# Kernel tuning notes

Measured on AMD Instinct MI355X. Metric: run time of the kernel, lower is better.

## Reference

```python
import jax, jax.numpy as jnp
import numpy as np

B, N, L, K = 32, 512, 8, 8


def setup_inputs() -> dict:
    key = jax.random.key(0)
    k1, k2 = jax.random.split(key)
    A = jax.random.normal(k1, (B, N, N), dtype=jnp.float32)
    A = 0.5 * (A + A.transpose(0, 2, 1))  # symmetric matrix, as in MMF use-case
    O_stack = jax.random.normal(k2, (L, B, K, K), dtype=jnp.float32)  # per-level KxK rotations
    rng = np.random.default_rng(0)
    idx = np.stack([np.sort(rng.choice(N, K, replace=False)) for _ in range(B * L)])
    indices = jnp.asarray(idx.reshape(B, L, K), dtype=jnp.int32)  # sorted, distinct per (b,l)
    wavelet = indices[:, :, 0]  # wavelet index is one of the selected indices per level
    return {"A": A, "O_stack": O_stack, "indices": indices, "wavelet": wavelet}


def reference(A, O_stack, indices, wavelet):
    Bz, Nz, _ = A.shape
    Lz = O_stack.shape[0]
    eye = jnp.eye(Nz, dtype=A.dtype)

    def build_U(idx, O):
        # identity except the KxK block at (idx_i, idx_j) replaced by O
        # (matches torch boolean-mask row-major fill since idx is sorted)
        return eye.at[idx[:, None], idx[None, :]].set(O)

    right = None
    for l in range(Lz):
        U = jax.vmap(build_U)(indices[:, l], O_stack[l])  # [B,N,N]
        right = U if l == 0 else U @ right
        A = U @ A @ U.transpose(0, 2, 1)

    # final masking: zero rows/cols of wavelet indices, keep diagonal
    active = jnp.ones((Bz, Nz), dtype=A.dtype).at[jnp.arange(Bz)[:, None], wavelet].set(0.0)
    left = active[:, :, None] * active[:, None, :]
    d = jnp.arange(Nz)
    left = left.at[:, d, d].set(1.0)
    D = A * left
    A_rec = right.transpose(0, 2, 1) @ D @ right
    return (A_rec, right, D)
```

## Files before the change

kernel.cpp:

```cpp
#include <hip/hip_runtime.h>

#define BATCH 32
#define NDIM 512
#define LNUM 8
#define KDIM 8

#define WS_PM     0
#define WS_ACT    640
#define WS_RAT    78976
#define WS_RDT    111744
#define WS_STRIDE 144512

#define LSTR 65
typedef float f4 __attribute__((ext_vector_type(4)));

__global__ __launch_bounds__(256) void k_prep(
    const float* __restrict__ A, const float* __restrict__ O,
    const int* __restrict__ indices, const int* __restrict__ wavelet,
    float* __restrict__ ws, float* __restrict__ out)
{
    const int b  = blockIdx.x;
    const int cy = blockIdx.y;
    const int tid = threadIdx.x;
    float* base = ws + (size_t)b * WS_STRIDE;
    const size_t seg = (size_t)BATCH*NDIM*NDIM;

    __shared__ float Wl[64*LSTR];
    __shared__ __align__(16) float Buf1[64*LSTR];
    __shared__ __align__(16) float Buf2[64*LSTR];
    __shared__ __align__(16) float Buf3[64*LSTR];
    __shared__ int   pml[NDIM];
    __shared__ float actl[NDIM];
    __shared__ float actS[64];
    __shared__ int   idxsh[64];
    __shared__ int   Ssh[64];
    __shared__ float Oall[LNUM*KDIM*KDIM];
    __shared__ int   s_sh;

    for (int t = tid; t < LNUM*KDIM*KDIM; t += 256) {
        int l = t >> 6, k = t & 63;
        Oall[t] = O[((size_t)l*BATCH + b)*(KDIM*KDIM) + k];
    }
    if (tid < 64) idxsh[tid] = indices[b*64 + tid];
    for (int n = tid; n < NDIM; n += 256) { pml[n] = -1; actl[n] = 1.f; }
    __syncthreads();

    const int wv = tid >> 6;
    const int ln = tid & 63;
    int s_reg = 0;

    if (wv == 0) {
        int n = idxsh[ln];
        bool first = true;
        for (int t = 0; t < ln; ++t) if (idxsh[t] == n) first = false;
        unsigned long long m = __ballot(first);
        int rank = __popcll(m & ((1ull << ln) - 1ull));
        s_reg = (int)__popcll(m);
        if (first) { pml[n] = rank; Ssh[rank] = n; }
        if (ln >= s_reg) Ssh[ln] = 0;
        if (ln < LNUM) actl[wavelet[b*LNUM + ln]] = 0.f;
        if (ln == 0) s_sh = s_reg;
    }
    __syncthreads();

    if (wv == 0) {
        actS[ln] = actl[Ssh[ln]];
        for (int rr = 0; rr < 64; ++rr)
            Wl[rr*LSTR + ln] = (rr == ln && rr < s_reg) ? 1.f : 0.f;
        for (int l = 0; l < LNUM; ++l) {
            int pr[KDIM];
            float wcol[KDIM], accv[KDIM];
            #pragma unroll
            for (int j = 0; j < KDIM; ++j) pr[j] = pml[idxsh[l*KDIM + j]];
            #pragma unroll
            for (int j = 0; j < KDIM; ++j) wcol[j] = Wl[pr[j]*LSTR + ln];
            #pragma unroll
            for (int i = 0; i < KDIM; ++i) {
                float a = 0.f;
                #pragma unroll
                for (int j = 0; j < KDIM; ++j)
                    a += Oall[l*64 + i*KDIM + j] * wcol[j];
                accv[i] = a;
            }
            #pragma unroll
            for (int i = 0; i < KDIM; ++i) Wl[pr[i]*LSTR + ln] = accv[i];
        }
    } else {
        if (cy < 8) {
            const int j0 = cy * 64;
            for (int t = tid - 64; t < 1024; t += 192) {
                int n = t >> 4, cc = t & 15;
                f4 v = ((const f4*)(A + ((size_t)b*NDIM + Ssh[n])*NDIM + j0))[cc];
                ((f4*)(Buf1 + n*64))[cc] = v;
            }
        } else {
            for (int t = tid - 64; t < 4096; t += 192) {
                int n = t >> 6, mm = t & 63;
                Buf1[n*LSTR + mm] = A[((size_t)b*NDIM + Ssh[n])*NDIM + Ssh[mm]];
            }
            int*   g_posmap = (int*)(base + WS_PM);
            float* g_act    = base + WS_ACT;
            for (int n = tid - 64; n < NDIM; n += 192) {
                g_posmap[n] = pml[n]; g_act[n] = actl[n];
            }
        }
    }
    __syncthreads();
    const int s = s_sh;

    if (cy < 8) {
        const int j0 = cy * 64;
        float* AS  = Buf1;
        float* RAt = Buf2;
        float* g_RAT = base + WS_RAT;
        float* g_RDT = base + WS_RDT;

        const int g = wv;
        const int j = ln;
        const int jg = j0 + j;
        const int pj = pml[jg];
        const float aj = actl[jg];
        float racc[16];

        #pragma unroll
        for (int k = 0; k < 16; ++k) racc[k] = 0.f;
        for (int n = 0; n < 64; ++n) {
            float av = AS[n*64 + j];
            #pragma unroll
            for (int k = 0; k < 16; ++k) racc[k] += Wl[(g*16 + k)*LSTR + n] * av;
        }
        #pragma unroll
        for (int k = 0; k < 16; ++k) RAt[(g*16 + k)*64 + j] = racc[k];
        {
            f4* dst = (f4*)(g_RAT + (size_t)jg*64 + g*16);
            #pragma unroll
            for (int q = 0; q < 4; ++q) {
                f4 v = { racc[4*q], racc[4*q+1], racc[4*q+2], racc[4*q+3] };
                dst[q] = v;
            }
        }
        if (pj < 0) {
            #pragma unroll
            for (int k = 0; k < 16; ++k) {
                int r = g*16 + k;
                if (r < s) {
                    size_t ro = ((size_t)b*NDIM + Ssh[r])*NDIM + jg;
                    out[2*seg + ro] = racc[k] * actS[r] * aj;
                    out[seg + ro]   = 0.f;
                }
            }
        }
        __syncthreads();

        #pragma unroll
        for (int k = 0; k < 16; ++k) racc[k] = 0.f;
        for (int n = 0; n < 64; ++n) {
            float dt = actS[n] * RAt[n*64 + j];
            #pragma unroll
            for (int k = 0; k < 16; ++k) racc[k] += Wl[n*LSTR + g*16 + k] * dt;
        }
        #pragma unroll
        for (int k = 0; k < 16; ++k) racc[k] *= aj;
        {
            f4* dst = (f4*)(g_RDT + (size_t)jg*64 + g*16);
            #pragma unroll
            for (int q = 0; q < 4; ++q) {
                f4 v = { racc[4*q], racc[4*q+1], racc[4*q+2], racc[4*q+3] };
                dst[q] = v;
            }
        }
        if (pj < 0) {
            #pragma unroll
            for (int k = 0; k < 16; ++k) {
                int r = g*16 + k;
                if (r < s) {
                    size_t ro = ((size_t)b*NDIM + Ssh[r])*NDIM + jg;
                    out[ro] = racc[k];
                }
            }
        }
    } else {
        const int w = wv;
        float acc[16];

        #pragma unroll
        for (int k = 0; k < 16; ++k) acc[k] = 0.f;
        for (int n = 0; n < 64; ++n) {
            float as = Buf1[n*LSTR + ln];
            #pragma unroll
            for (int k = 0; k < 16; ++k) acc[k] += Wl[(w*16 + k)*LSTR + n] * as;
        }
        #pragma unroll
        for (int k = 0; k < 16; ++k) Buf2[(w*16 + k)*LSTR + ln] = acc[k];
        __syncthreads();

        #pragma unroll
        for (int k = 0; k < 16; ++k) acc[k] = 0.f;
        for (int m = 0; m < 64; ++m) {
            float wvv = Wl[ln*LSTR + m];
            #pragma unroll
            for (int k = 0; k < 16; ++k) acc[k] += Buf2[(w*16 + k)*LSTR + m] * wvv;
        }
        #pragma unroll
        for (int k = 0; k < 16; ++k) Buf3[(w*16 + k)*LSTR + ln] = acc[k];
        __syncthreads();

        for (int t = tid; t < 4096; t += 256) {
            int n = t >> 6, m = t & 63;
            float mv = (Ssh[n] == Ssh[m]) ? 1.f : actS[n]*actS[m];
            Buf1[n*LSTR + m] = mv * Buf3[n*LSTR + m];
        }
        __syncthreads();

        #pragma unroll
        for (int k = 0; k < 16; ++k) acc[k] = 0.f;
        for (int n = 0; n < 64; ++n) {
            float dv = Buf1[n*LSTR + ln];
            #pragma unroll
            for (int k = 0; k < 16; ++k) acc[k] += Wl[n*LSTR + (w*16 + k)] * dv;
        }
        #pragma unroll
        for (int k = 0; k < 16; ++k) Buf2[(w*16 + k)*LSTR + ln] = acc[k];
        __syncthreads();

        #pragma unroll
        for (int k = 0; k < 16; ++k) acc[k] = 0.f;
        for (int m = 0; m < 64; ++m) {
            float wvv = Wl[m*LSTR + ln];
            #pragma unroll
            for (int k = 0; k < 16; ++k) acc[k] += Buf2[(w*16 + k)*LSTR + m] * wvv;
        }
        if (ln < s) {
            #pragma unroll
            for (int k = 0; k < 16; ++k) {
                int p = w*16 + k;
                if (p < s) {
                    size_t ro = ((size_t)b*NDIM + Ssh[p])*NDIM + Ssh[ln];
                    out[ro]         = acc[k];
                    out[seg + ro]   = Wl[p*LSTR + ln];
                    out[2*seg + ro] = Buf1[p*LSTR + ln];
                }
            }
        }
    }
}

__global__ __launch_bounds__(256) void k_big(const float* __restrict__ A,
                                             const float* __restrict__ ws,
                                             float* __restrict__ out)
{
    const int b = blockIdx.y;
    const int rh = threadIdx.x >> 7;
    const int lane = threadIdx.x & 127;
    const int j0 = lane*4;

    const float* base = ws + (size_t)b * WS_STRIDE;
    const int*   posmap = (const int*)(base + WS_PM);
    const float* act = base + WS_ACT;
    const float* RAT = base + WS_RAT;
    const float* RDT = base + WS_RDT;
    const size_t seg = (size_t)BATCH*NDIM*NDIM;
    const size_t brow = (size_t)b*NDIM;

    int4   p4  = ((const int4*)posmap)[lane];
    float4 aj4 = ((const float4*)act)[lane];
    const int   pm[4] = {p4.x, p4.y, p4.z, p4.w};
    const float aj[4] = {aj4.x, aj4.y, aj4.z, aj4.w};

    const int ibase = blockIdx.x*8 + rh;

    f4 vcur = __builtin_nontemporal_load(
        (const f4*)(A + (brow + ibase)*NDIM) + lane);

    #pragma unroll
    for (int it = 0; it < 4; ++it) {
        const int i = ibase + it*2;
        f4 v = vcur;
        if (it < 3) {
            vcur = __builtin_nontemporal_load(
                (const f4*)(A + (brow + i + 2)*NDIM) + lane);
        }
        const int pi = posmap[i];
        if (pi >= 0) continue;

        const float acti = act[i];
        const size_t rowoff = (brow + i)*NDIM;
        const float* rat = RAT + (size_t)i*64;
        const float* rdt = RDT + (size_t)i*64;

        float a[4], arec[4], dv[4], rv[4];
        a[0]=v.x; a[1]=v.y; a[2]=v.z; a[3]=v.w;
        #pragma unroll
        for (int c = 0; c < 4; ++c) {
            int pj = pm[c];
            if (pj >= 0) a[c] = rat[pj];
            float mv = (i == j0 + c) ? 1.f : acti * aj[c];
            dv[c] = a[c] * mv;
            arec[c] = (pj < 0) ? dv[c] : rdt[pj];
            rv[c] = (i == j0 + c) ? 1.f : 0.f;
        }

        f4 o0 = {arec[0], arec[1], arec[2], arec[3]};
        f4 o1 = {rv[0],   rv[1],   rv[2],   rv[3]};
        f4 o2 = {dv[0],   dv[1],   dv[2],   dv[3]};
        ((f4*)(out + rowoff))[lane]         = o0;
        ((f4*)(out + seg + rowoff))[lane]   = o1;
        ((f4*)(out + 2*seg + rowoff))[lane] = o2;
    }
}

extern "C" void kernel_launch(void* const* d_in, const int* in_sizes, int n_in,
                              void* d_out, int out_size, void* d_ws, size_t ws_size,
                              hipStream_t stream) {
    const float* A       = (const float*)d_in[0];
    const float* O       = (const float*)d_in[1];
    const int*   indices = (const int*)d_in[2];
    const int*   wavelet = (const int*)d_in[3];
    float* ws  = (float*)d_ws;
    float* out = (float*)d_out;

    k_prep<<<dim3(BATCH, 9), 256, 0, stream>>>(A, O, indices, wavelet, ws, out);
    k_big <<<dim3(NDIM/8, BATCH), 256, 0, stream>>>(A, ws, out);
}
```

Baseline: 173.6 us.

## Drop workspace by staging intermediates in the output buffer and recomputing maps

```diff
diff --git a/kernel.cpp b/kernel.cpp
--- a/kernel.cpp
+++ b/kernel.cpp
@@ -5,24 +5,17 @@
 #define LNUM 8
 #define KDIM 8
 
-#define WS_PM     0
-#define WS_ACT    640
-#define WS_RAT    78976
-#define WS_RDT    111744
-#define WS_STRIDE 144512
-
 #define LSTR 65
 typedef float f4 __attribute__((ext_vector_type(4)));
 
 __global__ __launch_bounds__(256) void k_prep(
     const float* __restrict__ A, const float* __restrict__ O,
     const int* __restrict__ indices, const int* __restrict__ wavelet,
-    float* __restrict__ ws, float* __restrict__ out)
+    float* __restrict__ out)
 {
     const int b  = blockIdx.x;
     const int cy = blockIdx.y;
     const int tid = threadIdx.x;
-    float* base = ws + (size_t)b * WS_STRIDE;
     const size_t seg = (size_t)BATCH*NDIM*NDIM;
 
     __shared__ float Wl[64*LSTR];
@@ -98,11 +91,6 @@
                 int n = t >> 6, mm = t & 63;
                 Buf1[n*LSTR + mm] = A[((size_t)b*NDIM + Ssh[n])*NDIM + Ssh[mm]];
             }
-            int*   g_posmap = (int*)(base + WS_PM);
-            float* g_act    = base + WS_ACT;
-            for (int n = tid - 64; n < NDIM; n += 192) {
-                g_posmap[n] = pml[n]; g_act[n] = actl[n];
-            }
         }
     }
     __syncthreads();
@@ -112,14 +100,13 @@
         const int j0 = cy * 64;
         float* AS  = Buf1;
         float* RAt = Buf2;
-        float* g_RAT = base + WS_RAT;
-        float* g_RDT = base + WS_RDT;
 
         const int g = wv;
         const int j = ln;
         const int jg = j0 + j;
         const int pj = pml[jg];
         const float aj = actl[jg];
+        f4* scr = (f4*)(out + seg + ((size_t)b*NDIM + jg)*NDIM);
         float racc[16];
 
         #pragma unroll
@@ -131,15 +118,12 @@
         }
         #pragma unroll
         for (int k = 0; k < 16; ++k) RAt[(g*16 + k)*64 + j] = racc[k];
-        {
-            f4* dst = (f4*)(g_RAT + (size_t)jg*64 + g*16);
+        if (pj < 0) {
             #pragma unroll
             for (int q = 0; q < 4; ++q) {
                 f4 v = { racc[4*q], racc[4*q+1], racc[4*q+2], racc[4*q+3] };
-                dst[q] = v;
-            }
-        }
-        if (pj < 0) {
+                scr[g*4 + q] = v;
+            }
             #pragma unroll
             for (int k = 0; k < 16; ++k) {
                 int r = g*16 + k;
@@ -161,15 +145,12 @@
         }
         #pragma unroll
         for (int k = 0; k < 16; ++k) racc[k] *= aj;
-        {
-            f4* dst = (f4*)(g_RDT + (size_t)jg*64 + g*16);
+        if (pj < 0) {
             #pragma unroll
             for (int q = 0; q < 4; ++q) {
                 f4 v = { racc[4*q], racc[4*q+1], racc[4*q+2], racc[4*q+3] };
-                dst[q] = v;
-            }
-        }
-        if (pj < 0) {
+                scr[16 + g*4 + q] = v;
+            }
             #pragma unroll
             for (int k = 0; k < 16; ++k) {
                 int r = g*16 + k;
@@ -246,31 +227,55 @@
 }
 
 __global__ __launch_bounds__(256) void k_big(const float* __restrict__ A,
-                                             const float* __restrict__ ws,
+                                             const int* __restrict__ indices,
+                                             const int* __restrict__ wavelet,
                                              float* __restrict__ out)
 {
     const int b = blockIdx.y;
-    const int rh = threadIdx.x >> 7;
-    const int lane = threadIdx.x & 127;
+    const int tid = threadIdx.x;
+    const int rh = tid >> 7;
+    const int lane = tid & 127;
     const int j0 = lane*4;
-
-    const float* base = ws + (size_t)b * WS_STRIDE;
-    const int*   posmap = (const int*)(base + WS_PM);
-    const float* act = base + WS_ACT;
-    const float* RAT = base + WS_RAT;
-    const float* RDT = base + WS_RDT;
     const size_t seg = (size_t)BATCH*NDIM*NDIM;
     const size_t brow = (size_t)b*NDIM;
-
-    int4   p4  = ((const int4*)posmap)[lane];
-    float4 aj4 = ((const float4*)act)[lane];
+    const int ibase0 = blockIdx.x*8;
+    const int ibase  = ibase0 + rh;
+
+    __shared__ __align__(16) int   pml[NDIM];
+    __shared__ __align__(16) float actl[NDIM];
+    __shared__ __align__(16) float ratl[8*64];
+    __shared__ __align__(16) float rdtl[8*64];
+    __shared__ int idxsh[64];
+
+    f4 vcur = __builtin_nontemporal_load(
+        (const f4*)(A + (brow + ibase)*NDIM) + lane);
+
+    for (int n = tid; n < NDIM; n += 256) { pml[n] = -1; actl[n] = 1.f; }
+    if (tid < 64) idxsh[tid] = indices[b*64 + tid];
+    {
+        const int u = tid >> 5, m = tid & 31;
+        f4 v = ((const f4*)(out + seg + (brow + ibase0 + u)*NDIM))[m];
+        float* dst = (m < 16) ? (ratl + u*64 + m*4) : (rdtl + u*64 + (m-16)*4);
+        *(f4*)dst = v;
+    }
+    __syncthreads();
+
+    if (tid < 64) {
+        const int ln = tid;
+        int n = idxsh[ln];
+        bool first = true;
+        for (int t = 0; t < ln; ++t) if (idxsh[t] == n) first = false;
+        unsigned long long m = __ballot(first);
+        int rank = __popcll(m & ((1ull << ln) - 1ull));
+        if (first) pml[n] = rank;
+        if (ln < LNUM) actl[wavelet[b*LNUM + ln]] = 0.f;
+    }
+    __syncthreads();
+
+    int4   p4  = ((const int4*)pml)[lane];
+    float4 aj4 = ((const float4*)actl)[lane];
     const int   pm[4] = {p4.x, p4.y, p4.z, p4.w};
     const float aj[4] = {aj4.x, aj4.y, aj4.z, aj4.w};
-
-    const int ibase = blockIdx.x*8 + rh;
-
-    f4 vcur = __builtin_nontemporal_load(
-        (const f4*)(A + (brow + ibase)*NDIM) + lane);
 
     #pragma unroll
     for (int it = 0; it < 4; ++it) {
@@ -280,13 +285,13 @@
             vcur = __builtin_nontemporal_load(
                 (const f4*)(A + (brow + i + 2)*NDIM) + lane);
         }
-        const int pi = posmap[i];
+        const int pi = pml[i];
         if (pi >= 0) continue;
 
-        const float acti = act[i];
+        const float acti = actl[i];
         const size_t rowoff = (brow + i)*NDIM;
-        const float* rat = RAT + (size_t)i*64;
-        const float* rdt = RDT + (size_t)i*64;
+        const float* rat = ratl + (rh + it*2)*64;
+        const float* rdt = rdtl + (rh + it*2)*64;
 
         float a[4], arec[4], dv[4], rv[4];
         a[0]=v.x; a[1]=v.y; a[2]=v.z; a[3]=v.w;
@@ -316,9 +321,9 @@
     const float* O       = (const float*)d_in[1];
     const int*   indices = (const int*)d_in[2];
     const int*   wavelet = (const int*)d_in[3];
-    float* ws  = (float*)d_ws;
     float* out = (float*)d_out;
-
-    k_prep<<<dim3(BATCH, 9), 256, 0, stream>>>(A, O, indices, wavelet, ws, out);
-    k_big <<<dim3(NDIM/8, BATCH), 256, 0, stream>>>(A, ws, out);
+    (void)d_ws; (void)ws_size;
+
+    k_prep<<<dim3(BATCH, 9), 256, 0, stream>>>(A, O, indices, wavelet, out);
+    k_big <<<dim3(NDIM/8, BATCH), 256, 0, stream>>>(A, indices, wavelet, out);
 }
```

Measured after the change: 171.0 us. Within noise of the previous version (-1.5%).
